# Optimization experiments

Hardware: AMD Instinct MI355X
Metric: run time of the kernel (lower is better)

The kernel has to match this reference:

```python
import jax, jax.numpy as jnp
import numpy as np

N = 100000   # nodes
E = 800000   # edges
D = 128      # input feature dim
H = 128      # hidden_channels
O = 64       # out_channels
L = 3        # num_layers
DROP_P = 0.5
NEG_SLOPE = 0.01  # F.leaky_relu default


def setup_inputs() -> dict:
    key = jax.random.key(0)
    ks = jax.random.split(key, 8)
    x = jax.random.normal(ks[0], (N, D), dtype=jnp.float32)
    edge_index = jax.random.randint(ks[1], (2, E), 0, N, dtype=jnp.int64)
    s = 1.0 / np.sqrt(D)
    Wl = jax.random.uniform(ks[2], (L, H, D), jnp.float32, -s, s)
    Wr = jax.random.uniform(ks[3], (L, H, D), jnp.float32, -s, s)
    b = jax.random.uniform(ks[4], (L, H), jnp.float32, -s, s)
    so = 1.0 / np.sqrt(H)
    Wo = jax.random.uniform(ks[5], (O, H), jnp.float32, -so, so)
    bo = jax.random.uniform(ks[6], (O,), jnp.float32, -so, so)
    return {"x": x, "edge_index": edge_index, "Wl": Wl, "Wr": Wr, "b": b, "Wo": Wo, "bo": bo}


def reference(x, edge_index, Wl, Wr, b, Wo, bo):
    src, dst = edge_index[0], edge_index[1]
    # in-degree counts for mean aggregation (computed once; graph is static)
    deg = jax.ops.segment_sum(jnp.ones((E,), x.dtype), dst, num_segments=N)
    inv_deg = jnp.where(deg > 0, 1.0 / jnp.maximum(deg, 1.0), 0.0)[:, None]  # [N,1]
    dkey = jax.random.key(42)
    for l in range(L):
        # SAGEConv: mean over incoming neighbor features, then two linears
        agg = jax.ops.segment_sum(x[src], dst, num_segments=N) * inv_deg  # [N,H]
        x = agg @ Wl[l].T + x @ Wr[l].T + b[l]
        x = jax.nn.leaky_relu(x, NEG_SLOPE)
        # dropout p=0.5 (training mode in torch F.dropout default); fixed keys
        keep = jax.random.bernoulli(jax.random.fold_in(dkey, l), 1.0 - DROP_P, x.shape)
        x = jnp.where(keep, x / (1.0 - DROP_P), 0.0)
    return x @ Wo.T + bo
```

## Files before the change

kernel.cpp:

```cpp
#include <hip/hip_runtime.h>
#include <cstdint>
#include <cstddef>

#define NN 100000
#define EE 800000
#define HD 128
#define OD 64
#define CAP 64
#define WPL 400000
#define ALDS 136

typedef __attribute__((ext_vector_type(8))) short s16x8;
typedef __attribute__((ext_vector_type(4))) float f32x4;
typedef __attribute__((ext_vector_type(8))) unsigned short u16x8;

__device__ __forceinline__ unsigned short f2bf(float f) {
  unsigned u = __float_as_uint(f);
  return (unsigned short)((u + 0x7FFFu + ((u >> 16) & 1u)) >> 16);
}
__device__ __forceinline__ float bf2f(unsigned short v) {
  return __uint_as_float(((unsigned)v) << 16);
}

__host__ __device__ __forceinline__ unsigned rotl32(unsigned x, int r) {
#ifdef __HIP_DEVICE_COMPILE__
  return __builtin_amdgcn_alignbit(x, x, 32 - r);
#else
  return (x << r) | (x >> (32 - r));
#endif
}

__host__ __device__ __forceinline__ void tf2x32(unsigned k0, unsigned k1,
                                                unsigned x0, unsigned x1,
                                                unsigned& o0, unsigned& o1) {
  unsigned ks2 = k0 ^ k1 ^ 0x1BD11BDAu;
#define TFR(r) { x0 += x1; x1 = rotl32(x1, (r)) ^ x0; }
  x0 += k0; x1 += k1;
  TFR(13) TFR(15) TFR(26) TFR(6)
  x0 += k1; x1 += ks2 + 1u;
  TFR(17) TFR(29) TFR(16) TFR(24)
  x0 += ks2; x1 += k0 + 2u;
  TFR(13) TFR(15) TFR(26) TFR(6)
  x0 += k0; x1 += k1 + 3u;
  TFR(17) TFR(29) TFR(16) TFR(24)
  x0 += k1; x1 += ks2 + 4u;
  TFR(13) TFR(15) TFR(26) TFR(6)
  x0 += ks2; x1 += k0 + 5u;
#undef TFR
  o0 = x0; o1 = x1;
}

__device__ __forceinline__ void gen_mask_1024(unsigned long long* __restrict__ maskW,
                                              int wave, int lane,
                                              unsigned k0, unsigned k1) {
  const unsigned base = (unsigned)wave * 1024u + (unsigned)lane;
#pragma unroll
  for (int c = 0; c < 16; ++c) {
    unsigned r0, r1;
    tf2x32(k0, k1, 0u, base + (unsigned)(c << 6), r0, r1);
    unsigned long long m = __ballot(((r0 ^ r1) & 0x80000000u) == 0u);
    if (lane == 0) maskW[wave * 16 + c] = m;
  }
}

__device__ __forceinline__ void cast8(const float* __restrict__ x,
                                      unsigned short* __restrict__ xb, int t) {
  const float4* p = (const float4*)x + (size_t)t * 2;
  float4 v0 = p[0], v1 = p[1];
  u16x8 r;
  r[0] = f2bf(v0.x); r[1] = f2bf(v0.y); r[2] = f2bf(v0.z); r[3] = f2bf(v0.w);
  r[4] = f2bf(v1.x); r[5] = f2bf(v1.y); r[6] = f2bf(v1.z); r[7] = f2bf(v1.w);
  *((u16x8*)xb + t) = r;
}

__global__ __launch_bounds__(256) void k_castw(const float* __restrict__ Wl,
                                               const float* __restrict__ Wr,
                                               const float* __restrict__ Wo,
                                               unsigned short* __restrict__ Wb,
                                               unsigned short* __restrict__ Wob) {
  int t = blockIdx.x * 256 + threadIdx.x;
  if (t < 3 * 128 * 256) {
    int l = t >> 15;
    int rem = t & 32767;
    int n = rem >> 8;
    int k = rem & 255;
    float w = (k < 128) ? Wl[(l << 14) + (n << 7) + k] : Wr[(l << 14) + (n << 7) + (k - 128)];
    int sw = rem ^ ((n & 7) << 3);
    Wb[(l << 15) + sw] = f2bf(w);
  } else {
    int t3 = t - 3 * 128 * 256;
    if (t3 < OD * 128) Wob[t3] = f2bf(Wo[t3]);
  }
}

__global__ __launch_bounds__(256) void k_fill2(const int* __restrict__ ei,
                                               int* __restrict__ fill,
                                               int* __restrict__ bucket,
                                               unsigned long long* __restrict__ mask1,
                                               unsigned mk0, unsigned mk1,
                                               const float* __restrict__ x,
                                               unsigned short* __restrict__ xb) {
  const int e = blockIdx.x * 256 + threadIdx.x;
  unsigned s = (unsigned)ei[e];
  unsigned d = (unsigned)ei[EE + e];
  if (s >= NN) s = 0;
  if (d >= NN) d = 0;
  int p = atomicAdd(&fill[d], 1);
  cast8(x, xb, e);
  cast8(x, xb, EE + e);
  gen_mask_1024(mask1, e >> 6, e & 63, mk0, mk1);
  if (p < CAP) bucket[d * CAP + p] = (int)s;
}

__global__ __launch_bounds__(256) void k_aggb(const unsigned short* __restrict__ xb,
                                              const int* __restrict__ bucket,
                                              const int* __restrict__ fill,
                                              unsigned short* __restrict__ aggb,
                                              unsigned long long* __restrict__ maskW,
                                              unsigned mk0, unsigned mk1) {
  const int w = (blockIdx.x * 256 + threadIdx.x) >> 6;
  const int lane = threadIdx.x & 63;
  const int q = lane >> 4;
  const int ql = lane & 15;
  const int qb = q << 4;
  const int n = (w << 2) + q;

  const int degf = fill[n];
  const int deg = (degf < CAP) ? degf : CAP;
  int idx = (ql < deg) ? bucket[n * CAP + ql] : 0;
  const float sc = (degf > 0) ? 1.0f / (float)degf : 0.0f;

  if (maskW) {
    const unsigned base = (unsigned)w * 512u + (unsigned)lane;
#pragma unroll
    for (int c = 0; c < 8; ++c) {
      unsigned r0, r1;
      tf2x32(mk0, mk1, 0u, base + (unsigned)(c << 6), r0, r1);
      unsigned long long m = __ballot(((r0 ^ r1) & 0x80000000u) == 0u);
      if (lane == 0) maskW[(w << 3) + c] = m;
    }
  }

  const u16x8* xb8 = (const u16x8*)xb;
  float a0[8], a1[8], a2[8], a3[8];
#pragma unroll
  for (int k = 0; k < 8; ++k) { a0[k] = 0.f; a1[k] = 0.f; a2[k] = 0.f; a3[k] = 0.f; }

  const int dcap = (deg < 16) ? deg : 16;
  int i0 = 0;
  for (; i0 + 4 <= dcap; i0 += 4) {
    int j0 = __shfl(idx, qb + i0);
    int j1 = __shfl(idx, qb + i0 + 1);
    int j2 = __shfl(idx, qb + i0 + 2);
    int j3 = __shfl(idx, qb + i0 + 3);
    u16x8 v0 = xb8[(size_t)j0 * 16 + ql];
    u16x8 v1 = xb8[(size_t)j1 * 16 + ql];
    u16x8 v2 = xb8[(size_t)j2 * 16 + ql];
    u16x8 v3 = xb8[(size_t)j3 * 16 + ql];
#pragma unroll
    for (int k = 0; k < 8; ++k) {
      a0[k] += bf2f(v0[k]); a1[k] += bf2f(v1[k]);
      a2[k] += bf2f(v2[k]); a3[k] += bf2f(v3[k]);
    }
  }
  {
    const int rem = dcap - i0;
    int j0 = __shfl(idx, qb + (i0 & 15));
    int j1 = __shfl(idx, qb + ((i0 + 1) & 15));
    int j2 = __shfl(idx, qb + ((i0 + 2) & 15));
    if (rem > 0) {
      u16x8 v = xb8[(size_t)j0 * 16 + ql];
#pragma unroll
      for (int k = 0; k < 8; ++k) a0[k] += bf2f(v[k]);
    }
    if (rem > 1) {
      u16x8 v = xb8[(size_t)j1 * 16 + ql];
#pragma unroll
      for (int k = 0; k < 8; ++k) a1[k] += bf2f(v[k]);
    }
    if (rem > 2) {
      u16x8 v = xb8[(size_t)j2 * 16 + ql];
#pragma unroll
      for (int k = 0; k < 8; ++k) a2[k] += bf2f(v[k]);
    }
  }
  for (int i = 16; i < deg; ++i) {
    int sX = bucket[n * CAP + i];
    u16x8 v = xb8[(size_t)sX * 16 + ql];
#pragma unroll
    for (int k = 0; k < 8; ++k) a3[k] += bf2f(v[k]);
  }

  u16x8 o;
#pragma unroll
  for (int k = 0; k < 8; ++k)
    o[k] = f2bf(((a0[k] + a1[k]) + (a2[k] + a3[k])) * sc);
  ((u16x8*)aggb)[(size_t)n * 16 + ql] = o;
}

__global__ __launch_bounds__(256) void k_layer_mfma(
    const unsigned short* __restrict__ xin,
    const unsigned short* __restrict__ aggb,
    const unsigned short* __restrict__ Wb,
    const float* __restrict__ bias,
    const unsigned* __restrict__ mask,
    unsigned short* __restrict__ xout) {
  __shared__ unsigned short Wlds[16384];
  const int tid = threadIdx.x;
  const int lane = tid & 63;
  const int wv = tid >> 6;
  const int rbase = blockIdx.x * 64 + wv * 16;
  const int lr = lane & 15;
  const int lkq = lane >> 4;
  const int rowg = lkq * 4;

  const f32x4* Wv = (const f32x4*)Wb;
  f32x4* dst = (f32x4*)Wlds;

  f32x4 acc[8];
#pragma unroll
  for (int j = 0; j < 8; ++j) acc[j] = (f32x4){0.f, 0.f, 0.f, 0.f};

  int n0 = rbase + lr;
  if (n0 >= NN) n0 = NN - 1;

  const char* WL = (const char*)Wlds;
#pragma unroll
  for (int half = 0; half < 2; ++half) {
    if (half) __syncthreads();
#pragma unroll
    for (int it = 0; it < 8; ++it) {
      const int c = it * 256 + tid;
      dst[c] = Wv[((c >> 4) << 5) + (half << 4) + (c & 15)];
    }
    __syncthreads();
    const unsigned short* A = half ? xin : aggb;
#pragma unroll
    for (int kfl = 0; kfl < 4; ++kfl) {
      const int kc = kfl * 32 + lkq * 8;
      s16x8 a0 = *(const s16x8*)(A + (size_t)n0 * 128 + kc);
#pragma unroll
      for (int nf = 0; nf < 8; ++nf) {
        const int row = nf * 16 + lr;
        const int bo = (row << 8) + ((((kfl << 6) + (lkq << 4)) ^ ((row & 7) << 4)));
        s16x8 wfr = *(const s16x8*)(WL + bo);
        acc[nf] = __builtin_amdgcn_mfma_f32_16x16x32_bf16(wfr, a0, acc[nf], 0, 0, 0);
      }
    }
  }

  const int node = rbase + lr;
  if (node < NN) {
    const unsigned mbase = (unsigned)node * 4u;
#pragma unroll
    for (int nf = 0; nf < 8; ++nf) {
      const int colb = nf * 16 + rowg;
      const float4 bv = *(const float4*)(bias + colb);
      const unsigned mw = mask[mbase + (colb >> 5)];
      const unsigned sh = (unsigned)(colb & 31);
      float v0 = acc[nf][0] + bv.x;
      float v1 = acc[nf][1] + bv.y;
      float v2 = acc[nf][2] + bv.z;
      float v3 = acc[nf][3] + bv.w;
      v0 = (v0 > 0.f) ? v0 : 0.01f * v0;
      v1 = (v1 > 0.f) ? v1 : 0.01f * v1;
      v2 = (v2 > 0.f) ? v2 : 0.01f * v2;
      v3 = (v3 > 0.f) ? v3 : 0.01f * v3;
      ushort4 o;
      o.x = ((mw >> (sh + 0)) & 1u) ? f2bf(v0 + v0) : (unsigned short)0;
      o.y = ((mw >> (sh + 1)) & 1u) ? f2bf(v1 + v1) : (unsigned short)0;
      o.z = ((mw >> (sh + 2)) & 1u) ? f2bf(v2 + v2) : (unsigned short)0;
      o.w = ((mw >> (sh + 3)) & 1u) ? f2bf(v3 + v3) : (unsigned short)0;
      *(ushort4*)(xout + (size_t)node * 128 + colb) = o;
    }
  }
}

__global__ __launch_bounds__(256) void k_layer3_final(
    const unsigned short* __restrict__ xin,
    const unsigned short* __restrict__ aggb,
    const unsigned short* __restrict__ Wb,
    const float* __restrict__ bias,
    const unsigned* __restrict__ mask,
    const unsigned short* __restrict__ Wob,
    const float* __restrict__ bo,
    float* __restrict__ out) {
  __shared__ unsigned short smem[16384];
  const int tid = threadIdx.x;
  const int lane = tid & 63;
  const int wv = tid >> 6;
  const int rbase = blockIdx.x * 64 + wv * 16;
  const int lr = lane & 15;
  const int lkq = lane >> 4;
  const int rowg = lkq * 4;

  const f32x4* Wv = (const f32x4*)Wb;
  f32x4* dst = (f32x4*)smem;

  f32x4 acc[8];
#pragma unroll
  for (int j = 0; j < 8; ++j) acc[j] = (f32x4){0.f, 0.f, 0.f, 0.f};

  int n0 = rbase + lr;
  if (n0 >= NN) n0 = NN - 1;

  const char* WL = (const char*)smem;
#pragma unroll
  for (int half = 0; half < 2; ++half) {
    if (half) __syncthreads();
#pragma unroll
    for (int it = 0; it < 8; ++it) {
      const int c = it * 256 + tid;
      dst[c] = Wv[((c >> 4) << 5) + (half << 4) + (c & 15)];
    }
    __syncthreads();
    const unsigned short* A = half ? xin : aggb;
#pragma unroll
    for (int kfl = 0; kfl < 4; ++kfl) {
      const int kc = kfl * 32 + lkq * 8;
      s16x8 a0 = *(const s16x8*)(A + (size_t)n0 * 128 + kc);
#pragma unroll
      for (int nf = 0; nf < 8; ++nf) {
        const int row = nf * 16 + lr;
        const int bo2 = (row << 8) + ((((kfl << 6) + (lkq << 4)) ^ ((row & 7) << 4)));
        s16x8 wfr = *(const s16x8*)(WL + bo2);
        acc[nf] = __builtin_amdgcn_mfma_f32_16x16x32_bf16(wfr, a0, acc[nf], 0, 0, 0);
      }
    }
  }

  __syncthreads();
  {
    const int node = rbase + lr;
    const int nodec = (node < NN) ? node : (NN - 1);
    const unsigned mbase = (unsigned)nodec * 4u;
    const int arow = wv * 16 + lr;
#pragma unroll
    for (int nf = 0; nf < 8; ++nf) {
      const int colb = nf * 16 + rowg;
      const float4 bv = *(const float4*)(bias + colb);
      const unsigned mw = mask[mbase + (colb >> 5)];
      const unsigned sh = (unsigned)(colb & 31);
      float v0 = acc[nf][0] + bv.x;
      float v1 = acc[nf][1] + bv.y;
      float v2 = acc[nf][2] + bv.z;
      float v3 = acc[nf][3] + bv.w;
      v0 = (v0 > 0.f) ? v0 : 0.01f * v0;
      v1 = (v1 > 0.f) ? v1 : 0.01f * v1;
      v2 = (v2 > 0.f) ? v2 : 0.01f * v2;
      v3 = (v3 > 0.f) ? v3 : 0.01f * v3;
      ushort4 o;
      o.x = ((mw >> (sh + 0)) & 1u) ? f2bf(v0 + v0) : (unsigned short)0;
      o.y = ((mw >> (sh + 1)) & 1u) ? f2bf(v1 + v1) : (unsigned short)0;
      o.z = ((mw >> (sh + 2)) & 1u) ? f2bf(v2 + v2) : (unsigned short)0;
      o.w = ((mw >> (sh + 3)) & 1u) ? f2bf(v3 + v3) : (unsigned short)0;
      *(ushort4*)(smem + arow * ALDS + colb) = o;
    }
  }
  __syncthreads();

  f32x4 acc2[4];
#pragma unroll
  for (int j = 0; j < 4; ++j) acc2[j] = (f32x4){0.f, 0.f, 0.f, 0.f};

  const int arow = wv * 16 + lr;
#pragma unroll
  for (int kf = 0; kf < 4; ++kf) {
    const int kc = kf * 32 + lkq * 8;
    s16x8 a0 = *(const s16x8*)(smem + arow * ALDS + kc);
#pragma unroll
    for (int nf = 0; nf < 4; ++nf) {
      s16x8 wfr = *(const s16x8*)(Wob + (nf * 16 + lr) * 128 + kc);
      acc2[nf] = __builtin_amdgcn_mfma_f32_16x16x32_bf16(wfr, a0, acc2[nf], 0, 0, 0);
    }
  }

  const int node = rbase + lr;
  if (node < NN) {
#pragma unroll
    for (int nf = 0; nf < 4; ++nf) {
      const int colb = nf * 16 + rowg;
      const float4 bv = *(const float4*)(bo + colb);
      float4 o;
      o.x = acc2[nf][0] + bv.x;
      o.y = acc2[nf][1] + bv.y;
      o.z = acc2[nf][2] + bv.z;
      o.w = acc2[nf][3] + bv.w;
      *(float4*)(out + (size_t)node * 64 + colb) = o;
    }
  }
}

extern "C" void kernel_launch(void* const* d_in, const int* in_sizes, int n_in,
                              void* d_out, int out_size, void* d_ws, size_t ws_size,
                              hipStream_t stream) {
  const float* x  = (const float*)d_in[0];
  const int*   ei = (const int*)d_in[1];
  const float* Wl = (const float*)d_in[2];
  const float* Wr = (const float*)d_in[3];
  const float* b  = (const float*)d_in[4];
  const float* Wo = (const float*)d_in[5];
  const float* bo = (const float*)d_in[6];
  float* out = (float*)d_out;

  char* wsp = (char*)d_ws;
  size_t off = 0;
  auto take = [&](size_t bytes) -> void* {
    off = (off + 255) & ~(size_t)255;
    void* p = wsp + off;
    off += bytes;
    return p;
  };
  unsigned short* xb0    = (unsigned short*)take((size_t)NN * 128 * 2);
  unsigned short* act1   = (unsigned short*)take((size_t)NN * 128 * 2);
  unsigned short* act2   = (unsigned short*)take((size_t)NN * 128 * 2);
  unsigned short* aggb   = (unsigned short*)take((size_t)NN * 128 * 2);
  unsigned short* Wb     = (unsigned short*)take((size_t)3 * 128 * 256 * 2);
  unsigned short* Wob    = (unsigned short*)take((size_t)OD * 128 * 2);
  unsigned*       masks  = (unsigned*)take((size_t)3 * WPL * 4);
  int*            bucket = (int*)take((size_t)NN * CAP * 4);
  int*            fill   = (int*)take((size_t)NN * 4);

  unsigned fk[3][2];
  for (int l = 0; l < 3; ++l) tf2x32(0u, 42u, 0u, (unsigned)l, fk[l][0], fk[l][1]);

  hipMemsetAsync(fill, 0, (size_t)NN * 4, stream);
  k_castw<<<(3 * 128 * 256 + OD * 128 + 255) / 256, 256, 0, stream>>>(Wl, Wr, Wo, Wb, Wob);
  k_fill2<<<EE / 256, 256, 0, stream>>>(ei, fill, bucket,
                                        (unsigned long long*)(masks + WPL),
                                        fk[1][0], fk[1][1], x, xb0);

  const int gemmBlocks = (NN + 63) / 64;
  const int aggBlocks  = 6250;

  k_aggb<<<aggBlocks, 256, 0, stream>>>(xb0, bucket, fill, aggb,
                                        (unsigned long long*)masks, fk[0][0], fk[0][1]);
  k_layer_mfma<<<gemmBlocks, 256, 0, stream>>>(xb0, aggb, Wb, b, masks, act1);

  k_aggb<<<aggBlocks, 256, 0, stream>>>(act1, bucket, fill, aggb,
                                        (unsigned long long*)(masks + 2 * WPL),
                                        fk[2][0], fk[2][1]);
  k_layer_mfma<<<gemmBlocks, 256, 0, stream>>>(act1, aggb, Wb + 32768, b + 128,
                                               masks + WPL, act2);

  k_aggb<<<aggBlocks, 256, 0, stream>>>(act2, bucket, fill, aggb,
                                        (unsigned long long*)0, 0u, 0u);
  k_layer3_final<<<gemmBlocks, 256, 0, stream>>>(act2, aggb, Wb + 65536, b + 256,
                                                 masks + 2 * WPL, Wob, bo, out);

  (void)in_sizes; (void)n_in; (void)out_size; (void)ws_size;
}
```

Before: 272.9 us.

## Fold weight cast into fill kernel, split mask gen, unroll gather by eight

Removes the separate weight-cast launch by doing the bf16 weight conversion inside the edge-fill kernel using the edge thread index. The layer-3 dropout mask generation is split across the second and third aggregation kernels to balance their work. The neighbor gather loop is unrolled to eight outstanding loads per step, with a generalized remainder path, to raise memory-level parallelism. The extra loads in flight may raise register pressure, and the mask loop now has a runtime trip count instead of a fixed unroll.

```diff
diff --git a/kernel.cpp b/kernel.cpp
--- a/kernel.cpp
+++ b/kernel.cpp
@@ -73,39 +73,36 @@
   *((u16x8*)xb + t) = r;
 }
 
-__global__ __launch_bounds__(256) void k_castw(const float* __restrict__ Wl,
-                                               const float* __restrict__ Wr,
-                                               const float* __restrict__ Wo,
-                                               unsigned short* __restrict__ Wb,
-                                               unsigned short* __restrict__ Wob) {
-  int t = blockIdx.x * 256 + threadIdx.x;
-  if (t < 3 * 128 * 256) {
-    int l = t >> 15;
-    int rem = t & 32767;
-    int n = rem >> 8;
-    int k = rem & 255;
-    float w = (k < 128) ? Wl[(l << 14) + (n << 7) + k] : Wr[(l << 14) + (n << 7) + (k - 128)];
-    int sw = rem ^ ((n & 7) << 3);
-    Wb[(l << 15) + sw] = f2bf(w);
-  } else {
-    int t3 = t - 3 * 128 * 256;
-    if (t3 < OD * 128) Wob[t3] = f2bf(Wo[t3]);
-  }
-}
-
 __global__ __launch_bounds__(256) void k_fill2(const int* __restrict__ ei,
                                                int* __restrict__ fill,
                                                int* __restrict__ bucket,
                                                unsigned long long* __restrict__ mask1,
                                                unsigned mk0, unsigned mk1,
                                                const float* __restrict__ x,
-                                               unsigned short* __restrict__ xb) {
+                                               unsigned short* __restrict__ xb,
+                                               const float* __restrict__ Wl,
+                                               const float* __restrict__ Wr,
+                                               const float* __restrict__ Wo,
+                                               unsigned short* __restrict__ Wb,
+                                               unsigned short* __restrict__ Wob) {
   const int e = blockIdx.x * 256 + threadIdx.x;
   unsigned s = (unsigned)ei[e];
   unsigned d = (unsigned)ei[EE + e];
   if (s >= NN) s = 0;
   if (d >= NN) d = 0;
   int p = atomicAdd(&fill[d], 1);
+  if (e < 3 * 128 * 256) {
+    int l = e >> 15;
+    int rem = e & 32767;
+    int n = rem >> 8;
+    int k = rem & 255;
+    float w = (k < 128) ? Wl[(l << 14) + (n << 7) + k] : Wr[(l << 14) + (n << 7) + (k - 128)];
+    int sw = rem ^ ((n & 7) << 3);
+    Wb[(l << 15) + sw] = f2bf(w);
+  } else if (e < 3 * 128 * 256 + OD * 128) {
+    int t3 = e - 3 * 128 * 256;
+    Wob[t3] = f2bf(Wo[t3]);
+  }
   cast8(x, xb, e);
   cast8(x, xb, EE + e);
   gen_mask_1024(mask1, e >> 6, e & 63, mk0, mk1);
@@ -117,7 +114,8 @@
                                               const int* __restrict__ fill,
                                               unsigned short* __restrict__ aggb,
                                               unsigned long long* __restrict__ maskW,
-                                              unsigned mk0, unsigned mk1) {
+                                              unsigned mk0, unsigned mk1,
+                                              int mcBase, int mcCnt) {
   const int w = (blockIdx.x * 256 + threadIdx.x) >> 6;
   const int lane = threadIdx.x & 63;
   const int q = lane >> 4;
@@ -131,13 +129,12 @@
   const float sc = (degf > 0) ? 1.0f / (float)degf : 0.0f;
 
   if (maskW) {
-    const unsigned base = (unsigned)w * 512u + (unsigned)lane;
-#pragma unroll
-    for (int c = 0; c < 8; ++c) {
+    for (int c = 0; c < mcCnt; ++c) {
+      const int cc = mcBase + c;
       unsigned r0, r1;
-      tf2x32(mk0, mk1, 0u, base + (unsigned)(c << 6), r0, r1);
+      tf2x32(mk0, mk1, 0u, (unsigned)w * 512u + (unsigned)(cc << 6) + (unsigned)lane, r0, r1);
       unsigned long long m = __ballot(((r0 ^ r1) & 0x80000000u) == 0u);
-      if (lane == 0) maskW[(w << 3) + c] = m;
+      if (lane == 0) maskW[(w << 3) + cc] = m;
     }
   }
 
@@ -148,40 +145,39 @@
 
   const int dcap = (deg < 16) ? deg : 16;
   int i0 = 0;
-  for (; i0 + 4 <= dcap; i0 += 4) {
-    int j0 = __shfl(idx, qb + i0);
-    int j1 = __shfl(idx, qb + i0 + 1);
-    int j2 = __shfl(idx, qb + i0 + 2);
-    int j3 = __shfl(idx, qb + i0 + 3);
-    u16x8 v0 = xb8[(size_t)j0 * 16 + ql];
-    u16x8 v1 = xb8[(size_t)j1 * 16 + ql];
-    u16x8 v2 = xb8[(size_t)j2 * 16 + ql];
-    u16x8 v3 = xb8[(size_t)j3 * 16 + ql];
+  for (; i0 + 8 <= dcap; i0 += 8) {
+    int j[8];
+#pragma unroll
+    for (int t = 0; t < 8; ++t) j[t] = __shfl(idx, qb + i0 + t);
+    u16x8 v0 = xb8[(size_t)j[0] * 16 + ql];
+    u16x8 v1 = xb8[(size_t)j[1] * 16 + ql];
+    u16x8 v2 = xb8[(size_t)j[2] * 16 + ql];
+    u16x8 v3 = xb8[(size_t)j[3] * 16 + ql];
+    u16x8 v4 = xb8[(size_t)j[4] * 16 + ql];
+    u16x8 v5 = xb8[(size_t)j[5] * 16 + ql];
+    u16x8 v6 = xb8[(size_t)j[6] * 16 + ql];
+    u16x8 v7 = xb8[(size_t)j[7] * 16 + ql];
 #pragma unroll
     for (int k = 0; k < 8; ++k) {
-      a0[k] += bf2f(v0[k]); a1[k] += bf2f(v1[k]);
-      a2[k] += bf2f(v2[k]); a3[k] += bf2f(v3[k]);
+      a0[k] += bf2f(v0[k]) + bf2f(v4[k]);
+      a1[k] += bf2f(v1[k]) + bf2f(v5[k]);
+      a2[k] += bf2f(v2[k]) + bf2f(v6[k]);
+      a3[k] += bf2f(v3[k]) + bf2f(v7[k]);
     }
   }
   {
     const int rem = dcap - i0;
-    int j0 = __shfl(idx, qb + (i0 & 15));
-    int j1 = __shfl(idx, qb + ((i0 + 1) & 15));
-    int j2 = __shfl(idx, qb + ((i0 + 2) & 15));
-    if (rem > 0) {
-      u16x8 v = xb8[(size_t)j0 * 16 + ql];
-#pragma unroll
-      for (int k = 0; k < 8; ++k) a0[k] += bf2f(v[k]);
-    }
-    if (rem > 1) {
-      u16x8 v = xb8[(size_t)j1 * 16 + ql];
-#pragma unroll
-      for (int k = 0; k < 8; ++k) a1[k] += bf2f(v[k]);
-    }
-    if (rem > 2) {
-      u16x8 v = xb8[(size_t)j2 * 16 + ql];
-#pragma unroll
-      for (int k = 0; k < 8; ++k) a2[k] += bf2f(v[k]);
+    int j[7];
+#pragma unroll
+    for (int t = 0; t < 7; ++t) j[t] = __shfl(idx, qb + ((i0 + t) & 15));
+#pragma unroll
+    for (int t = 0; t < 7; ++t) {
+      if (t < rem) {
+        u16x8 v = xb8[(size_t)j[t] * 16 + ql];
+        float* a = (t & 3) == 0 ? a0 : ((t & 3) == 1 ? a1 : ((t & 3) == 2 ? a2 : a3));
+#pragma unroll
+        for (int k = 0; k < 8; ++k) a[k] += bf2f(v[k]);
+      }
     }
   }
   for (int i = 16; i < deg; ++i) {
@@ -425,26 +421,28 @@
   for (int l = 0; l < 3; ++l) tf2x32(0u, 42u, 0u, (unsigned)l, fk[l][0], fk[l][1]);
 
   hipMemsetAsync(fill, 0, (size_t)NN * 4, stream);
-  k_castw<<<(3 * 128 * 256 + OD * 128 + 255) / 256, 256, 0, stream>>>(Wl, Wr, Wo, Wb, Wob);
   k_fill2<<<EE / 256, 256, 0, stream>>>(ei, fill, bucket,
                                         (unsigned long long*)(masks + WPL),
-                                        fk[1][0], fk[1][1], x, xb0);
+                                        fk[1][0], fk[1][1], x, xb0,
+                                        Wl, Wr, Wo, Wb, Wob);
 
   const int gemmBlocks = (NN + 63) / 64;
   const int aggBlocks  = 6250;
 
   k_aggb<<<aggBlocks, 256, 0, stream>>>(xb0, bucket, fill, aggb,
-                                        (unsigned long long*)masks, fk[0][0], fk[0][1]);
+                                        (unsigned long long*)masks,
+                                        fk[0][0], fk[0][1], 0, 8);
   k_layer_mfma<<<gemmBlocks, 256, 0, stream>>>(xb0, aggb, Wb, b, masks, act1);
 
   k_aggb<<<aggBlocks, 256, 0, stream>>>(act1, bucket, fill, aggb,
                                         (unsigned long long*)(masks + 2 * WPL),
-                                        fk[2][0], fk[2][1]);
+                                        fk[2][0], fk[2][1], 0, 4);
   k_layer_mfma<<<gemmBlocks, 256, 0, stream>>>(act1, aggb, Wb + 32768, b + 128,
                                                masks + WPL, act2);
 
   k_aggb<<<aggBlocks, 256, 0, stream>>>(act2, bucket, fill, aggb,
-                                        (unsigned long long*)0, 0u, 0u);
+                                        (unsigned long long*)(masks + 2 * WPL),
+                                        fk[2][0], fk[2][1], 4, 4);
   k_layer3_final<<<gemmBlocks, 256, 0, stream>>>(act2, aggb, Wb + 65536, b + 256,
                                                  masks + 2 * WPL, Wob, bo, out);
 
```

After: 303.9 us. +11.3%, slower.
